# Kernel tuning notes

Hardware: AMD Instinct MI355X
Metric: run time of the kernel (lower is better)

The kernel has to match this reference:

```python
import jax, jax.numpy as jnp
import numpy as np

B, N, D = 4, 2048, 512
H, DH = 8, 64
MLP = 2048
EPS = 1e-5


def setup_inputs() -> dict:
    key = jax.random.key(0)
    ks = jax.random.split(key, 8)
    s = lambda fan_in: 1.0 / np.sqrt(fan_in)
    return {
        "x": jax.random.normal(ks[0], (B, N, D), jnp.float32),
        "ln1_g": jnp.ones((D,), jnp.float32),
        "ln1_b": jnp.zeros((D,), jnp.float32),
        "Wqkv": jax.random.normal(ks[1], (D, 3 * H * DH), jnp.float32) * s(D),
        "temperature": jnp.asarray(np.log(DH ** -0.5), jnp.float32),
        "Wo": jax.random.normal(ks[2], (H * DH, D), jnp.float32) * s(H * DH),
        "bo": jnp.zeros((D,), jnp.float32),
        "ln2_g": jnp.ones((D,), jnp.float32),
        "ln2_b": jnp.zeros((D,), jnp.float32),
        "W1": jax.random.normal(ks[3], (D, MLP), jnp.float32) * s(D),
        "b1": jnp.zeros((MLP,), jnp.float32),
        "W2": jax.random.normal(ks[4], (MLP, D), jnp.float32) * s(MLP),
        "b2": jnp.zeros((D,), jnp.float32),
    }


def _layernorm(x, g, b):
    mu = jnp.mean(x, axis=-1, keepdims=True)
    var = jnp.var(x, axis=-1, keepdims=True)
    return (x - mu) * jax.lax.rsqrt(var + EPS) * g + b


def _lsa(x, Wqkv, temperature, Wo, bo):
    b, n, _ = x.shape
    qkv = x @ Wqkv  # [b, n, 3*H*DH]
    q, k, v = jnp.split(qkv, 3, axis=-1)
    rs = lambda t: t.reshape(b, n, H, DH).transpose(0, 2, 1, 3)  # b h n d
    q, k, v = rs(q), rs(k), rs(v)
    dots = jnp.einsum("bhnd,bhmd->bhnm", q, k) * jnp.exp(temperature)
    mask_value = -jnp.finfo(dots.dtype).max
    eye = jnp.eye(n, dtype=bool)
    dots = jnp.where(eye, mask_value, dots)  # mask diagonal (LSA)
    attn = jax.nn.softmax(dots, axis=-1)
    out = jnp.einsum("bhnm,bhmd->bhnd", attn, v)
    out = out.transpose(0, 2, 1, 3).reshape(b, n, H * DH)
    return out @ Wo + bo


def _ffn(x, W1, b1, W2, b2):
    h = jax.nn.gelu(x @ W1 + b1, approximate=False)
    return h @ W2 + b2


def reference(x, ln1_g, ln1_b, Wqkv, temperature, Wo, bo,
              ln2_g, ln2_b, W1, b1, W2, b2):
    y = _lsa(_layernorm(x, ln1_g, ln1_b), Wqkv, temperature, Wo, bo) + x
    z = _ffn(_layernorm(y, ln2_g, ln2_b), W1, b1, W2, b2) + y
    return (z, x)
```

## Files before the change

### kernel.cpp

```cpp
#include <hip/hip_runtime.h>
#include <math.h>

typedef __attribute__((ext_vector_type(4))) float f32x4;
typedef __attribute__((ext_vector_type(8))) short short8;

#define DEV __device__ __forceinline__

DEV short f2bf(float f){
  union { float f; unsigned u; } v; v.f = f;
  unsigned r = v.u + 0x7fffu + ((v.u >> 16) & 1u);
  return (short)(r >> 16);
}
DEV float bf2f(short s){
  union { unsigned u; float f; } v; v.u = ((unsigned)(unsigned short)s) << 16; return v.f;
}
DEV float exp2_hw(float x){ float r; asm("v_exp_f32 %0, %1" : "=v"(r) : "v"(x)); return r; }
DEV float rcp_hw(float x){ float r; asm("v_rcp_f32 %0, %1" : "=v"(r) : "v"(x)); return r; }
DEV unsigned cvtpk(float a, float b){
  unsigned r; asm("v_cvt_pk_bf16_f32 %0, %1, %2" : "=v"(r) : "v"(a), "v"(b)); return r;
}
DEV void gload_lds16(const short* src, short* lds){
  __builtin_amdgcn_global_load_lds(
      (const __attribute__((address_space(1))) void*)src,
      (__attribute__((address_space(3))) void*)lds, 16, 0, 0);
}
DEV float gelu_fast(float v){
  float u = v * (0.79788456f + 0.03567741f * v * v);
  float e = exp2_hw(u * 2.88539008f);
  float th = 1.0f - 2.0f * rcp_hw(e + 1.0f);
  return 0.5f * v * (1.0f + th);
}

__global__ __launch_bounds__(256) void prep_kernel(
    const float* __restrict__ Wqkv, short* __restrict__ wqkv_t,
    const float* __restrict__ Wo,   short* __restrict__ wo_t,
    const float* __restrict__ W1,   short* __restrict__ w1_t,
    const float* __restrict__ W2,   short* __restrict__ w2_t,
    const float* __restrict__ x, const float* __restrict__ ln1g,
    const float* __restrict__ ln1b, short* __restrict__ h,
    float* __restrict__ xcopy)
{
  int bid = blockIdx.x;
  if (bid < 3072) {
    const float* W; short* Wt; int K, N, nbx, local;
    if (bid < 768)       { W = Wqkv; Wt = wqkv_t; K = 512;  N = 1536; nbx = 48; local = bid; }
    else if (bid < 1024) { W = Wo;   Wt = wo_t;   K = 512;  N = 512;  nbx = 16; local = bid - 768; }
    else if (bid < 2048) { W = W1;   Wt = w1_t;   K = 512;  N = 2048; nbx = 64; local = bid - 1024; }
    else                 { W = W2;   Wt = w2_t;   K = 2048; N = 512;  nbx = 16; local = bid - 2048; }
    __shared__ float tile[32][33];
    int nb = (local % nbx) * 32, kb = (local / nbx) * 32;
    int tx = threadIdx.x & 31, ty = threadIdx.x >> 5;
    #pragma unroll
    for (int i = ty; i < 32; i += 8)
      tile[i][tx] = W[(size_t)(kb + i) * N + nb + tx];
    __syncthreads();
    #pragma unroll
    for (int i = ty; i < 32; i += 8)
      Wt[(size_t)(nb + i) * K + kb + tx] = f2bf(tile[tx][i]);
    return;
  }
  int row  = (bid - 3072) * 4 + (threadIdx.x >> 6);
  int lane = threadIdx.x & 63;
  const float* xr = x + (size_t)row * 512 + lane * 8;
  f32x4 v0 = *(const f32x4*)(xr);
  f32x4 v1 = *(const f32x4*)(xr + 4);
  float s  = (v0[0]+v0[1]+v0[2]+v0[3]) + (v1[0]+v1[1]+v1[2]+v1[3]);
  float sq = (v0[0]*v0[0]+v0[1]*v0[1]+v0[2]*v0[2]+v0[3]*v0[3])
           + (v1[0]*v1[0]+v1[1]*v1[1]+v1[2]*v1[2]+v1[3]*v1[3]);
  #pragma unroll
  for (int off = 1; off < 64; off <<= 1) {
    s  += __shfl_xor(s, off);
    sq += __shfl_xor(sq, off);
  }
  float mu  = s * (1.0f / 512.0f);
  float var = sq * (1.0f / 512.0f) - mu * mu;
  float rstd = rsqrtf(var + 1e-5f);
  f32x4 g0 = *(const f32x4*)(ln1g + lane * 8);
  f32x4 g1 = *(const f32x4*)(ln1g + lane * 8 + 4);
  f32x4 b0 = *(const f32x4*)(ln1b + lane * 8);
  f32x4 b1 = *(const f32x4*)(ln1b + lane * 8 + 4);
  float o[8];
  #pragma unroll
  for (int j = 0; j < 4; ++j) o[j]     = (v0[j] - mu) * rstd * g0[j] + b0[j];
  #pragma unroll
  for (int j = 0; j < 4; ++j) o[4 + j] = (v1[j] - mu) * rstd * g1[j] + b1[j];
  uint4 pk;
  pk.x = cvtpk(o[0], o[1]); pk.y = cvtpk(o[2], o[3]);
  pk.z = cvtpk(o[4], o[5]); pk.w = cvtpk(o[6], o[7]);
  *(uint4*)(h + (size_t)row * 512 + lane * 8) = pk;
  float* xc = xcopy + (size_t)row * 512 + lane * 8;
  *(f32x4*)(xc)     = v0;
  *(f32x4*)(xc + 4) = v1;
}

__global__ __launch_bounds__(256) void ln_bf_kernel(
    const short* __restrict__ x, const float* __restrict__ g,
    const float* __restrict__ b, short* __restrict__ out)
{
  int row  = blockIdx.x * 4 + (threadIdx.x >> 6);
  int lane = threadIdx.x & 63;
  short8 raw = *(const short8*)(x + (size_t)row * 512 + lane * 8);
  float v[8];
  #pragma unroll
  for (int j = 0; j < 8; ++j) v[j] = bf2f(raw[j]);
  float s = 0.f, sq = 0.f;
  #pragma unroll
  for (int j = 0; j < 8; ++j) { s += v[j]; sq += v[j] * v[j]; }
  #pragma unroll
  for (int off = 1; off < 64; off <<= 1) {
    s  += __shfl_xor(s, off);
    sq += __shfl_xor(sq, off);
  }
  float mu  = s * (1.0f / 512.0f);
  float var = sq * (1.0f / 512.0f) - mu * mu;
  float rstd = rsqrtf(var + 1e-5f);
  f32x4 g0 = *(const f32x4*)(g + lane * 8);
  f32x4 g1 = *(const f32x4*)(g + lane * 8 + 4);
  f32x4 b0 = *(const f32x4*)(b + lane * 8);
  f32x4 b1 = *(const f32x4*)(b + lane * 8 + 4);
  float o[8];
  #pragma unroll
  for (int j = 0; j < 4; ++j) o[j]     = (v[j] - mu) * rstd * g0[j] + b0[j];
  #pragma unroll
  for (int j = 0; j < 4; ++j) o[4 + j] = (v[4+j] - mu) * rstd * g1[j] + b1[j];
  uint4 pk;
  pk.x = cvtpk(o[0], o[1]); pk.y = cvtpk(o[2], o[3]);
  pk.z = cvtpk(o[4], o[5]); pk.w = cvtpk(o[6], o[7]);
  *(uint4*)(out + (size_t)row * 512 + lane * 8) = pk;
}

template<int EPI, int BM, typename OutT>
__global__ __launch_bounds__(256) void gemm_bt_kernel(
    const short* __restrict__ A, const short* __restrict__ Bt,
    OutT* __restrict__ C, const float* __restrict__ bias,
    const float* __restrict__ resid, const short* __restrict__ residb,
    int M, int N, int K)
{
  constexpr int MFR = BM / 32;
  constexpr int NFR = 4;
  constexpr int AI  = BM / 32;
  constexpr int BUF = (BM + 128) * 64;
  __shared__ __align__(16) short smem[3 * BUF];

  int tid = threadIdx.x;
  int lane = tid & 63, wid = tid >> 6;
  int l16 = lane & 15, lq = lane >> 4;

  int gx = gridDim.x;
  int nwg = gx * gridDim.y;
  int orig = blockIdx.y * gx + blockIdx.x;
  int swz = (orig & 7) * (nwg >> 3) + (orig >> 3);
  int bn = swz % gx, bm = swz / gx;

  int wm = wid >> 1, wn = wid & 1;

  const short* gaP[AI];
  const short* gbP[4];
  #pragma unroll
  for (int i = 0; i < AI; ++i) {
    int g = i * 4 + wid;
    gaP[i] = A + (size_t)(bm * BM + (g >> 1) * 16 + l16) * K + (g & 1) * 32 + lq * 8;
  }
  #pragma unroll
  for (int i = 0; i < 4; ++i) {
    int g = i * 4 + wid;
    gbP[i] = Bt + (size_t)(bn * 128 + (g >> 1) * 16 + l16) * K + (g & 1) * 32 + lq * 8;
  }

  auto STAGE = [&](int bufi, int k0) {
    short* base = smem + bufi * BUF;
    #pragma unroll
    for (int i = 0; i < AI; ++i)
      gload_lds16(gaP[i] + k0, base + (i * 4 + wid) * 512);
    #pragma unroll
    for (int i = 0; i < 4; ++i)
      gload_lds16(gbP[i] + k0, base + BM * 64 + (i * 4 + wid) * 512);
  };

  f32x4 acc[MFR][NFR] = {};

  STAGE(0, 0);
  STAGE(1, 64);

  int nt = K >> 6;
  for (int t = 0; t < nt; ++t) {
    if (t + 1 < nt) asm volatile("s_waitcnt vmcnt(6)" ::: "memory");
    else            asm volatile("s_waitcnt vmcnt(0)" ::: "memory");
    __builtin_amdgcn_s_barrier();
    __builtin_amdgcn_sched_barrier(0);
    if (t + 2 < nt) STAGE((t + 2) % 3, (t + 2) << 6);

    const short* base = smem + (t % 3) * BUF;
    #pragma unroll
    for (int kc = 0; kc < 2; ++kc) {
      short8 af[MFR], bfr[NFR];
      #pragma unroll
      for (int m = 0; m < MFR; ++m)
        af[m] = *(const short8*)(base + ((wm * MFR + m) * 2 + kc) * 512 + lane * 8);
      #pragma unroll
      for (int n = 0; n < NFR; ++n)
        bfr[n] = *(const short8*)(base + BM * 64 + ((wn * NFR + n) * 2 + kc) * 512 + lane * 8);
      __builtin_amdgcn_s_setprio(1);
      #pragma unroll
      for (int m = 0; m < MFR; ++m)
        #pragma unroll
        for (int n = 0; n < NFR; ++n)
          acc[m][n] = __builtin_amdgcn_mfma_f32_16x16x32_bf16(af[m], bfr[n], acc[m][n], 0, 0, 0);
      __builtin_amdgcn_s_setprio(0);
    }
  }

  float bv[NFR];
  #pragma unroll
  for (int n = 0; n < NFR; ++n)
    bv[n] = bias[bn * 128 + (wn * NFR + n) * 16 + l16];

  #pragma unroll
  for (int m = 0; m < MFR; ++m) {
    #pragma unroll
    for (int r = 0; r < 4; ++r) {
      int row = bm * BM + (wm * MFR + m) * 16 + lq * 4 + r;
      #pragma unroll
      for (int n = 0; n < NFR; ++n) {
        int col = bn * 128 + (wn * NFR + n) * 16 + l16;
        float v = acc[m][n][r] + bv[n];
        if (EPI == 4) v += resid[(size_t)row * N + col];
        if (EPI == 5) v += bf2f(residb[(size_t)row * N + col]);
        if constexpr (sizeof(OutT) == 2)
          ((short*)C)[(size_t)row * N + col] = f2bf(v);
        else
          ((float*)C)[(size_t)row * N + col] = v;
      }
    }
  }
}

template<int EPI>
__global__ __launch_bounds__(512) void gemm256_kernel(
    const short* __restrict__ A, const short* __restrict__ Bt,
    short* __restrict__ C, const float* __restrict__ bias,
    short* __restrict__ vt, int M, int N, int K)
{
  constexpr int BUF = 24576;
  __shared__ __align__(16) short smem[3 * BUF];

  int tid = threadIdx.x;
  int lane = tid & 63, wid = tid >> 6;
  int l16 = lane & 15, lq = lane >> 4;

  int gx = gridDim.x;
  int nwg = gx * gridDim.y;
  int orig = blockIdx.y * gx + blockIdx.x;
  int swz = (orig & 7) * (nwg >> 3) + (orig >> 3);
  int bn = swz % gx, bm = swz / gx;

  int wm = wid >> 1, wn = wid & 1;

  const short* gaP[4];
  const short* gbP[2];
  #pragma unroll
  for (int i = 0; i < 4; ++i) {
    int g = i * 8 + wid;
    gaP[i] = A + (size_t)(bm * 256 + (g >> 1) * 16 + l16) * K + (g & 1) * 32 + lq * 8;
  }
  #pragma unroll
  for (int i = 0; i < 2; ++i) {
    int g = i * 8 + wid;
    gbP[i] = Bt + (size_t)(bn * 128 + (g >> 1) * 16 + l16) * K + (g & 1) * 32 + lq * 8;
  }

  auto STAGE = [&](int bufi, int k0) {
    short* base = smem + bufi * BUF;
    #pragma unroll
    for (int i = 0; i < 4; ++i)
      gload_lds16(gaP[i] + k0, base + (i * 8 + wid) * 512);
    #pragma unroll
    for (int i = 0; i < 2; ++i)
      gload_lds16(gbP[i] + k0, base + 16384 + (i * 8 + wid) * 512);
  };

  f32x4 acc[4][4] = {};

  STAGE(0, 0);
  STAGE(1, 64);

  int nt = K >> 6;
  for (int t = 0; t < nt; ++t) {
    if (t + 1 < nt) asm volatile("s_waitcnt vmcnt(6)" ::: "memory");
    else            asm volatile("s_waitcnt vmcnt(0)" ::: "memory");
    __builtin_amdgcn_s_barrier();
    __builtin_amdgcn_sched_barrier(0);
    if (t + 2 < nt) STAGE((t + 2) % 3, (t + 2) << 6);

    const short* base = smem + (t % 3) * BUF;
    #pragma unroll
    for (int kc = 0; kc < 2; ++kc) {
      short8 af[4], bfr[4];
      #pragma unroll
      for (int m = 0; m < 4; ++m)
        af[m] = *(const short8*)(base + ((wm * 4 + m) * 2 + kc) * 512 + lane * 8);
      #pragma unroll
      for (int n = 0; n < 4; ++n)
        bfr[n] = *(const short8*)(base + 16384 + ((wn * 4 + n) * 2 + kc) * 512 + lane * 8);
      __builtin_amdgcn_s_setprio(1);
      #pragma unroll
      for (int m = 0; m < 4; ++m)
        #pragma unroll
        for (int n = 0; n < 4; ++n)
          acc[m][n] = __builtin_amdgcn_mfma_f32_16x16x32_bf16(af[m], bfr[n], acc[m][n], 0, 0, 0);
      __builtin_amdgcn_s_setprio(0);
    }
  }

  if (EPI == 3 && bn >= 8) {
    __syncthreads();
    short* T = smem;
    #pragma unroll
    for (int m = 0; m < 4; ++m)
      #pragma unroll
      for (int n = 0; n < 4; ++n) {
        int c = wn * 64 + n * 16 + l16;
        #pragma unroll
        for (int r = 0; r < 4; ++r) {
          int rowl = wm * 64 + m * 16 + lq * 4 + r;
          T[c * 256 + (rowl ^ ((c & 7) << 4))] = f2bf(acc[m][n][r]);
        }
      }
    __syncthreads();
    int b2 = bm >> 3;
    int nnb = (bm & 7) * 256;
    int tn = tid & 31, cw = tid >> 5;
    #pragma unroll
    for (int c8 = 0; c8 < 8; ++c8) {
      int c = c8 * 16 + cw;
      short8 v = *(const short8*)(T + c * 256 + ((tn * 8) ^ ((c & 7) << 4)));
      if (tn & 1) {
        short8 w;
        #pragma unroll
        for (int j = 0; j < 8; ++j) w[j] = v[j ^ 4];
        v = w;
      }
      int c2 = bn * 128 + c - 1024;
      int bh = b2 * 8 + (c2 >> 6);
      int d  = c2 & 63;
      *(short8*)(vt + ((size_t)(bh * 64 + d)) * 2048 + nnb + tn * 8) = v;
    }
    return;
  }

  #pragma unroll
  for (int m = 0; m < 4; ++m) {
    #pragma unroll
    for (int r = 0; r < 4; ++r) {
      int row = bm * 256 + (wm * 4 + m) * 16 + lq * 4 + r;
      #pragma unroll
      for (int n = 0; n < 4; ++n) {
        int col = bn * 128 + (wn * 4 + n) * 16 + l16;
        C[(size_t)row * N + col] = f2bf(acc[m][n][r]);
      }
    }
  }
}

__global__ __launch_bounds__(512, 2) void gemm8p_kernel(
    const short* __restrict__ A, const short* __restrict__ Bt,
    short* __restrict__ C, const float* __restrict__ bias,
    int M, int N, int K)
{
  __shared__ __align__(16) short smem[2 * 32768];

  int tid = threadIdx.x;
  int lane = tid & 63, wid = tid >> 6;
  int l16 = lane & 15, lq = lane >> 4;
  int wm = wid >> 2, wn = wid & 3;

  int gx = gridDim.x;
  int nwg = gx * gridDim.y;
  int orig = blockIdx.y * gx + blockIdx.x;
  int swz = (orig & 7) * (nwg >> 3) + (orig >> 3);
  int bn = swz % gx, bm = swz / gx;

  const short* gaP[4];
  const short* gbP[4];
  #pragma unroll
  for (int i = 0; i < 4; ++i) {
    int idx = i * 512 + tid;
    int g = idx >> 6, ln = idx & 63;
    gaP[i] = A  + (size_t)(bm * 256 + (g >> 1) * 16 + (ln & 15)) * K
                + (g & 1) * 32 + (ln >> 4) * 8;
    gbP[i] = Bt + (size_t)(bn * 256 + (g >> 1) * 16 + (ln & 15)) * K
                + (g & 1) * 32 + (ln >> 4) * 8;
  }

  auto STAGE_A = [&](int buf, int k0) {
    short* dst = smem + buf * 32768;
    #pragma unroll
    for (int i = 0; i < 4; ++i)
      gload_lds16(gaP[i] + k0, dst + ((size_t)(i * 512 + tid)) * 8);
  };
  auto STAGE_B_LO = [&](int buf, int k0) {
    short* dst = smem + buf * 32768 + 16384;
    #pragma unroll
    for (int i = 0; i < 2; ++i)
      gload_lds16(gbP[i] + k0, dst + ((size_t)(i * 512 + tid)) * 8);
  };
  auto STAGE_B_HI = [&](int buf, int k0) {
    short* dst = smem + buf * 32768 + 16384;
    #pragma unroll
    for (int i = 2; i < 4; ++i)
      gload_lds16(gbP[i] + k0, dst + ((size_t)(i * 512 + tid)) * 8);
  };

  f32x4 acc[8][4] = {};

  STAGE_A(0, 0);
  STAGE_B_LO(0, 0); STAGE_B_HI(0, 0);
  STAGE_B_LO(1, 64); STAGE_B_HI(1, 64);
  asm volatile("s_waitcnt vmcnt(4)" ::: "memory");
  __builtin_amdgcn_s_barrier();

  int nt = K >> 6;
  for (int t = 0; t < nt; ++t) {
    int cur = t & 1;
    const short* As_ = smem + cur * 32768;
    const short* Bs_ = As_ + 16384;
    short8 bf[4][2];

    #pragma unroll
    for (int p = 0; p < 4; ++p) {
      short8 af[2][2];
      #pragma unroll
      for (int mm = 0; mm < 2; ++mm)
        #pragma unroll
        for (int kc = 0; kc < 2; ++kc)
          af[mm][kc] = *(const short8*)(As_ + ((wm * 8 + 2 * p + mm) * 2 + kc) * 512 + lane * 8);
      if (p == 0) {
        #pragma unroll
        for (int n = 0; n < 4; ++n)
          #pragma unroll
          for (int kc = 0; kc < 2; ++kc)
            bf[n][kc] = *(const short8*)(Bs_ + ((wn * 4 + n) * 2 + kc) * 512 + lane * 8);
      }
      if (p == 0 && t + 1 < nt) STAGE_A(cur ^ 1, (t + 1) << 6);
      if (p == 1 && t + 2 < nt) STAGE_B_LO(cur, (t + 2) << 6);
      if (p == 2 && t + 2 < nt) STAGE_B_HI(cur, (t + 2) << 6);

      __builtin_amdgcn_s_barrier();
      asm volatile("s_waitcnt lgkmcnt(0)" ::: "memory");
      __builtin_amdgcn_sched_barrier(0);
      __builtin_amdgcn_s_setprio(1);
      #pragma unroll
      for (int mm = 0; mm < 2; ++mm)
        #pragma unroll
        for (int n = 0; n < 4; ++n)
          #pragma unroll
          for (int kc = 0; kc < 2; ++kc)
            acc[2 * p + mm][n] = __builtin_amdgcn_mfma_f32_16x16x32_bf16(
                af[mm][kc], bf[n][kc], acc[2 * p + mm][n], 0, 0, 0);
      __builtin_amdgcn_s_setprio(0);
      if (p < 3) {
        __builtin_amdgcn_s_barrier();
      } else {
        if (t + 2 < nt) asm volatile("s_waitcnt vmcnt(4)" ::: "memory");
        else            asm volatile("s_waitcnt vmcnt(0)" ::: "memory");
        __builtin_amdgcn_s_barrier();
      }
    }
  }

  float bv[4];
  #pragma unroll
  for (int n = 0; n < 4; ++n)
    bv[n] = bias[bn * 256 + (wn * 4 + n) * 16 + l16];
  #pragma unroll
  for (int m = 0; m < 8; ++m) {
    #pragma unroll
    for (int r = 0; r < 4; ++r) {
      int row = bm * 256 + wm * 128 + m * 16 + lq * 4 + r;
      #pragma unroll
      for (int n = 0; n < 4; ++n) {
        int col = bn * 256 + (wn * 4 + n) * 16 + l16;
        C[(size_t)row * N + col] = f2bf(gelu_fast(acc[m][n][r] + bv[n]));
      }
    }
  }
}

__global__ __launch_bounds__(512, 4) void attn_kernel(
    const short* __restrict__ qkv, const short* __restrict__ vt,
    const float* __restrict__ temp_ptr,
    short* __restrict__ Op0, short* __restrict__ Op1, float* __restrict__ Lbuf)
{
  __shared__ __align__(16) short smem[16384];

  int tid = threadIdx.x;
  int lane = tid & 63, wid = tid >> 6;
  int l16 = lane & 15, lq = lane >> 4;
  int hi = lq >> 1, lq0 = lq & 1;

  int orig = blockIdx.y * 8 + blockIdx.x;
  int swz = (orig & 7) * 64 + (orig >> 3);
  int qb = swz & 7;
  int rr = swz >> 3;
  int bh = rr & 31, slice = rr >> 5;
  int b = bh >> 3, h = bh & 7;

  const short* qbase = qkv + (size_t)b * 2048 * 1536 + h * 64;
  const short* kbase = qbase + 512;
  const short* vbase = vt + (size_t)bh * 64 * 2048;
  int kslice = slice * 1024;

  float scale = __expf(temp_ptr[0]) * 1.44269504f;
  int q0 = qb * 256 + wid * 32;

  short8 qfrag[2][2];
  #pragma unroll
  for (int qf = 0; qf < 2; ++qf) {
    int qrow = q0 + qf * 16 + l16;
    #pragma unroll
    for (int c = 0; c < 2; ++c) {
      short8 raw = *(const short8*)(qbase + (size_t)qrow * 1536 + c * 32 + lq * 8);
      short8 sc;
      #pragma unroll
      for (int j = 0; j < 8; ++j) sc[j] = f2bf(bf2f(raw[j]) * scale);
      qfrag[qf][c] = sc;
    }
  }

  f32x4 accO[2][4] = {};
  float l[2] = {0.f, 0.f};

  auto STAGE = [&](int bufi, int k0) {
    int sub = wid >> 1, cc = wid & 1;
    const short* srcK = kbase + (size_t)(k0 + sub * 16 + l16) * 1536 + cc * 32 + lq * 8;
    gload_lds16(srcK, smem + bufi * 4096 + wid * 512);
    const short* srcV = vbase + (size_t)(sub * 16 + l16) * 2048 + k0 + cc * 32 + lq * 8;
    gload_lds16(srcV, smem + 8192 + bufi * 4096 + wid * 512);
  };

  STAGE(0, kslice);
  asm volatile("s_waitcnt vmcnt(0)");
  __syncthreads();

  for (int t = 0; t < 16; ++t) {
    int cur = t & 1;
    int k0 = kslice + t * 64;
    if (t + 1 < 16) STAGE(cur ^ 1, k0 + 64);

    const short* kls = smem + cur * 4096;
    const short* vls = smem + 8192 + cur * 4096;

    f32x4 accS[2][4] = {};
    #pragma unroll
    for (int s = 0; s < 4; ++s) {
      short8 kf0 = *(const short8*)(kls + (s * 2 + 0) * 512 + lane * 8);
      short8 kf1 = *(const short8*)(kls + (s * 2 + 1) * 512 + lane * 8);
      #pragma unroll
      for (int qf = 0; qf < 2; ++qf) {
        accS[qf][s] = __builtin_amdgcn_mfma_f32_16x16x32_bf16(kf0, qfrag[qf][0], accS[qf][s], 0, 0, 0);
        accS[qf][s] = __builtin_amdgcn_mfma_f32_16x16x32_bf16(kf1, qfrag[qf][1], accS[qf][s], 0, 0, 0);
      }
    }

    if ((q0 & ~63) == k0) {
      #pragma unroll
      for (int qf = 0; qf < 2; ++qf) {
        int qg = q0 + qf * 16 + l16;
        #pragma unroll
        for (int s = 0; s < 4; ++s)
          #pragma unroll
          for (int r = 0; r < 4; ++r)
            if (k0 + s * 16 + lq * 4 + r == qg) accS[qf][s][r] = -30000.f;
      }
    }

    short8 pa[2][2];
    #pragma unroll
    for (int qf = 0; qf < 2; ++qf) {
      float sum = 0.f;
      unsigned W[4][2];
      #pragma unroll
      for (int s = 0; s < 4; ++s) {
        float p0 = exp2_hw(accS[qf][s][0]);
        float p1 = exp2_hw(accS[qf][s][1]);
        float p2 = exp2_hw(accS[qf][s][2]);
        float p3 = exp2_hw(accS[qf][s][3]);
        sum += (p0 + p1) + (p2 + p3);
        W[s][0] = cvtpk(p0, p1);
        W[s][1] = cvtpk(p2, p3);
      }
      sum += __shfl_xor(sum, 16);
      sum += __shfl_xor(sum, 32);
      l[qf] += sum;

      unsigned K0[2], S0[2], K2[2], S2[2], R0[2], R2[2];
      #pragma unroll
      for (int w = 0; w < 2; ++w) {
        K0[w] = hi ? W[1][w] : W[0][w];
        S0[w] = hi ? W[0][w] : W[1][w];
        K2[w] = hi ? W[3][w] : W[2][w];
        S2[w] = hi ? W[2][w] : W[3][w];
      }
      #pragma unroll
      for (int w = 0; w < 2; ++w) {
        R0[w] = (unsigned)__shfl_xor((int)S0[w], 32);
        R2[w] = (unsigned)__shfl_xor((int)S2[w], 32);
      }
      bool sw = (hi != lq0);
      unsigned FA[2], FB[2], sA[2], sB[2], GA[2], GB[2];
      #pragma unroll
      for (int w = 0; w < 2; ++w) {
        sA[w] = sw ? K0[w] : R0[w];  FA[w] = sw ? R0[w] : K0[w];
        sB[w] = sw ? K2[w] : R2[w];  FB[w] = sw ? R2[w] : K2[w];
      }
      #pragma unroll
      for (int w = 0; w < 2; ++w) {
        GA[w] = (unsigned)__shfl_xor((int)sA[w], 16);
        GB[w] = (unsigned)__shfl_xor((int)sB[w], 16);
      }
      union { unsigned u[4]; short8 s8; } p0u, p1u;
      p0u.u[0] = FA[0]; p0u.u[1] = FA[1]; p0u.u[2] = GA[0]; p0u.u[3] = GA[1];
      p1u.u[0] = FB[0]; p1u.u[1] = FB[1]; p1u.u[2] = GB[0]; p1u.u[3] = GB[1];
      pa[qf][0] = p0u.s8;
      pa[qf][1] = p1u.s8;
    }

    short8 vfr[4][2];
    #pragma unroll
    for (int d = 0; d < 4; ++d) {
      vfr[d][0] = *(const short8*)(vls + (d * 2 + 0) * 512 + lane * 8);
      vfr[d][1] = *(const short8*)(vls + (d * 2 + 1) * 512 + lane * 8);
    }
    #pragma unroll
    for (int qf = 0; qf < 2; ++qf)
      #pragma unroll
      for (int d = 0; d < 4; ++d) {
        accO[qf][d] = __builtin_amdgcn_mfma_f32_16x16x32_bf16(vfr[d][0], pa[qf][0], accO[qf][d], 0, 0, 0);
        accO[qf][d] = __builtin_amdgcn_mfma_f32_16x16x32_bf16(vfr[d][1], pa[qf][1], accO[qf][d], 0, 0, 0);
      }

    __syncthreads();
  }

  short* op = slice ? Op1 : Op0;
  #pragma unroll
  for (int qf = 0; qf < 2; ++qf) {
    int qg = q0 + qf * 16 + l16;
    if (lq == 0) Lbuf[(size_t)(slice * 32 + bh) * 2048 + qg] = l[qf];
    size_t rowoff = (size_t)(b * 2048 + qg) * 512 + h * 64;
    #pragma unroll
    for (int d = 0; d < 4; ++d) {
      unsigned w0 = cvtpk(accO[qf][d][0], accO[qf][d][1]);
      unsigned w1 = cvtpk(accO[qf][d][2], accO[qf][d][3]);
      uint2 pk; pk.x = w0; pk.y = w1;
      *(uint2*)(op + rowoff + d * 16 + lq * 4) = pk;
    }
  }
}

__global__ __launch_bounds__(256) void attn_combine_kernel(
    const short* __restrict__ Op0, const short* __restrict__ Op1,
    const float* __restrict__ Lbuf, short* __restrict__ out)
{
  int idx = blockIdx.x * 256 + threadIdx.x;
  size_t e = (size_t)idx * 8;
  int row = (int)(e >> 9);
  int col = (int)(e & 511);
  int b = row >> 11, q = row & 2047;
  int bh = b * 8 + (col >> 6);
  float l0 = Lbuf[(size_t)bh * 2048 + q];
  float l1 = Lbuf[(size_t)(32 + bh) * 2048 + q];
  float inv = rcp_hw(l0 + l1);
  short8 a = *(const short8*)(Op0 + e);
  short8 c = *(const short8*)(Op1 + e);
  float o[8];
  #pragma unroll
  for (int j = 0; j < 8; ++j) o[j] = (bf2f(a[j]) + bf2f(c[j])) * inv;
  uint4 pk;
  pk.x = cvtpk(o[0], o[1]); pk.y = cvtpk(o[2], o[3]);
  pk.z = cvtpk(o[4], o[5]); pk.w = cvtpk(o[6], o[7]);
  *(uint4*)(out + e) = pk;
}

extern "C" void kernel_launch(void* const* d_in, const int* in_sizes, int n_in,
                              void* d_out, int out_size, void* d_ws, size_t ws_size,
                              hipStream_t stream)
{
  const float* x    = (const float*)d_in[0];
  const float* ln1g = (const float*)d_in[1];
  const float* ln1b = (const float*)d_in[2];
  const float* Wqkv = (const float*)d_in[3];
  const float* temp = (const float*)d_in[4];
  const float* Wo   = (const float*)d_in[5];
  const float* bo   = (const float*)d_in[6];
  const float* ln2g = (const float*)d_in[7];
  const float* ln2b = (const float*)d_in[8];
  const float* W1   = (const float*)d_in[9];
  const float* b1   = (const float*)d_in[10];
  const float* W2   = (const float*)d_in[11];
  const float* b2   = (const float*)d_in[12];
  float* out = (float*)d_out;

  char* ws = (char*)d_ws;
  short* wqkv_t = (short*)(ws);
  float* lpart  = (float*)(ws);
  short* wo_t   = (short*)(ws + 1572864);
  short* w1_t   = (short*)(ws + 2097152);
  short* w2_t   = (short*)(ws + 4194304);
  short* h      = (short*)(ws + 6291456);
  short* qkv    = (short*)(ws + 14680064);
  short* attn   = (short*)(ws + 39845888);
  short* ybf    = (short*)(ws + 48234496);
  short* vt     = (short*)(ws + 48234496);
  short* t      = (short*)(ws + 14680064);

  const int M = 8192;

  prep_kernel<<<3072 + 2048, 256, 0, stream>>>(
      Wqkv, wqkv_t, Wo, wo_t, W1, w1_t, W2, w2_t,
      x, ln1g, ln1b, h, out + (size_t)M * 512);

  gemm256_kernel<3><<<dim3(1536 / 128, M / 256), 512, 0, stream>>>(
      h, wqkv_t, qkv, nullptr, vt, M, 1536, 512);

  attn_kernel<<<dim3(8, 64), 512, 0, stream>>>(qkv, vt, temp, attn, h, lpart);
  attn_combine_kernel<<<M * 512 / 8 / 256, 256, 0, stream>>>(attn, h, lpart, attn);

  gemm_bt_kernel<4, 64, short><<<dim3(512 / 128, M / 64), 256, 0, stream>>>(
      attn, wo_t, ybf, bo, x, nullptr, M, 512, 512);

  ln_bf_kernel<<<M / 4, 256, 0, stream>>>(ybf, ln2g, ln2b, h);

  gemm8p_kernel<<<dim3(2048 / 256, M / 256), 512, 0, stream>>>(
      h, w1_t, t, b1, M, 2048, 512);

  gemm_bt_kernel<5, 64, float><<<dim3(512 / 128, M / 64), 256, 0, stream>>>(
      t, w2_t, out, b2, nullptr, ybf, M, 512, 2048);
}
```

Before: 191.8 us.

## Use 256x256 GEMM for QKV and split attention keys into four slices

The QKV projection now runs through the templated 256x256 eight-phase GEMM, which writes V transposed through its LDS epilogue, instead of the separate 256x128 kernel. Attention splits the key range into four slices instead of two, doubling the grid so more blocks stay resident per CU. The fourth partial output is stored in the now-unused V columns of the qkv buffer, and the combine kernel sums four partials. The trade-offs are that the QKV GEMM grid shrinks to 192 blocks, which may underfill the GPU, and the combine step now reads twice as much partial data.

```diff
diff --git a/kernel.cpp b/kernel.cpp
--- a/kernel.cpp
+++ b/kernel.cpp
@@ -235,137 +235,11 @@
   }
 }
 
-template<int EPI>
-__global__ __launch_bounds__(512) void gemm256_kernel(
+template<int QKV>
+__global__ __launch_bounds__(512, 2) void gemm8p_kernel(
     const short* __restrict__ A, const short* __restrict__ Bt,
     short* __restrict__ C, const float* __restrict__ bias,
     short* __restrict__ vt, int M, int N, int K)
-{
-  constexpr int BUF = 24576;
-  __shared__ __align__(16) short smem[3 * BUF];
-
-  int tid = threadIdx.x;
-  int lane = tid & 63, wid = tid >> 6;
-  int l16 = lane & 15, lq = lane >> 4;
-
-  int gx = gridDim.x;
-  int nwg = gx * gridDim.y;
-  int orig = blockIdx.y * gx + blockIdx.x;
-  int swz = (orig & 7) * (nwg >> 3) + (orig >> 3);
-  int bn = swz % gx, bm = swz / gx;
-
-  int wm = wid >> 1, wn = wid & 1;
-
-  const short* gaP[4];
-  const short* gbP[2];
-  #pragma unroll
-  for (int i = 0; i < 4; ++i) {
-    int g = i * 8 + wid;
-    gaP[i] = A + (size_t)(bm * 256 + (g >> 1) * 16 + l16) * K + (g & 1) * 32 + lq * 8;
-  }
-  #pragma unroll
-  for (int i = 0; i < 2; ++i) {
-    int g = i * 8 + wid;
-    gbP[i] = Bt + (size_t)(bn * 128 + (g >> 1) * 16 + l16) * K + (g & 1) * 32 + lq * 8;
-  }
-
-  auto STAGE = [&](int bufi, int k0) {
-    short* base = smem + bufi * BUF;
-    #pragma unroll
-    for (int i = 0; i < 4; ++i)
-      gload_lds16(gaP[i] + k0, base + (i * 8 + wid) * 512);
-    #pragma unroll
-    for (int i = 0; i < 2; ++i)
-      gload_lds16(gbP[i] + k0, base + 16384 + (i * 8 + wid) * 512);
-  };
-
-  f32x4 acc[4][4] = {};
-
-  STAGE(0, 0);
-  STAGE(1, 64);
-
-  int nt = K >> 6;
-  for (int t = 0; t < nt; ++t) {
-    if (t + 1 < nt) asm volatile("s_waitcnt vmcnt(6)" ::: "memory");
-    else            asm volatile("s_waitcnt vmcnt(0)" ::: "memory");
-    __builtin_amdgcn_s_barrier();
-    __builtin_amdgcn_sched_barrier(0);
-    if (t + 2 < nt) STAGE((t + 2) % 3, (t + 2) << 6);
-
-    const short* base = smem + (t % 3) * BUF;
-    #pragma unroll
-    for (int kc = 0; kc < 2; ++kc) {
-      short8 af[4], bfr[4];
-      #pragma unroll
-      for (int m = 0; m < 4; ++m)
-        af[m] = *(const short8*)(base + ((wm * 4 + m) * 2 + kc) * 512 + lane * 8);
-      #pragma unroll
-      for (int n = 0; n < 4; ++n)
-        bfr[n] = *(const short8*)(base + 16384 + ((wn * 4 + n) * 2 + kc) * 512 + lane * 8);
-      __builtin_amdgcn_s_setprio(1);
-      #pragma unroll
-      for (int m = 0; m < 4; ++m)
-        #pragma unroll
-        for (int n = 0; n < 4; ++n)
-          acc[m][n] = __builtin_amdgcn_mfma_f32_16x16x32_bf16(af[m], bfr[n], acc[m][n], 0, 0, 0);
-      __builtin_amdgcn_s_setprio(0);
-    }
-  }
-
-  if (EPI == 3 && bn >= 8) {
-    __syncthreads();
-    short* T = smem;
-    #pragma unroll
-    for (int m = 0; m < 4; ++m)
-      #pragma unroll
-      for (int n = 0; n < 4; ++n) {
-        int c = wn * 64 + n * 16 + l16;
-        #pragma unroll
-        for (int r = 0; r < 4; ++r) {
-          int rowl = wm * 64 + m * 16 + lq * 4 + r;
-          T[c * 256 + (rowl ^ ((c & 7) << 4))] = f2bf(acc[m][n][r]);
-        }
-      }
-    __syncthreads();
-    int b2 = bm >> 3;
-    int nnb = (bm & 7) * 256;
-    int tn = tid & 31, cw = tid >> 5;
-    #pragma unroll
-    for (int c8 = 0; c8 < 8; ++c8) {
-      int c = c8 * 16 + cw;
-      short8 v = *(const short8*)(T + c * 256 + ((tn * 8) ^ ((c & 7) << 4)));
-      if (tn & 1) {
-        short8 w;
-        #pragma unroll
-        for (int j = 0; j < 8; ++j) w[j] = v[j ^ 4];
-        v = w;
-      }
-      int c2 = bn * 128 + c - 1024;
-      int bh = b2 * 8 + (c2 >> 6);
-      int d  = c2 & 63;
-      *(short8*)(vt + ((size_t)(bh * 64 + d)) * 2048 + nnb + tn * 8) = v;
-    }
-    return;
-  }
-
-  #pragma unroll
-  for (int m = 0; m < 4; ++m) {
-    #pragma unroll
-    for (int r = 0; r < 4; ++r) {
-      int row = bm * 256 + (wm * 4 + m) * 16 + lq * 4 + r;
-      #pragma unroll
-      for (int n = 0; n < 4; ++n) {
-        int col = bn * 128 + (wn * 4 + n) * 16 + l16;
-        C[(size_t)row * N + col] = f2bf(acc[m][n][r]);
-      }
-    }
-  }
-}
-
-__global__ __launch_bounds__(512, 2) void gemm8p_kernel(
-    const short* __restrict__ A, const short* __restrict__ Bt,
-    short* __restrict__ C, const float* __restrict__ bias,
-    int M, int N, int K)
 {
   __shared__ __align__(16) short smem[2 * 32768];
 
@@ -468,10 +342,48 @@
     }
   }
 
+  if (QKV == 1 && bn >= 4) {
+    __syncthreads();
+    short* T = smem;
+    #pragma unroll
+    for (int m = 0; m < 8; ++m)
+      #pragma unroll
+      for (int n = 0; n < 4; ++n) {
+        int c = (wn * 4 + n) * 16 + l16;
+        #pragma unroll
+        for (int r = 0; r < 4; ++r) {
+          int rowl = wm * 128 + m * 16 + lq * 4 + r;
+          T[c * 256 + (rowl ^ ((c & 7) << 4))] = f2bf(acc[m][n][r]);
+        }
+      }
+    __syncthreads();
+    int b2 = bm >> 3;
+    int nnb = (bm & 7) * 256;
+    int tn = tid & 31, cw = tid >> 5;
+    #pragma unroll
+    for (int c8 = 0; c8 < 16; ++c8) {
+      int c = c8 * 16 + cw;
+      short8 v = *(const short8*)(T + c * 256 + ((tn * 8) ^ ((c & 7) << 4)));
+      if (tn & 1) {
+        short8 w;
+        #pragma unroll
+        for (int j = 0; j < 8; ++j) w[j] = v[j ^ 4];
+        v = w;
+      }
+      int c2 = bn * 256 + c - 1024;
+      int bh = b2 * 8 + (c2 >> 6);
+      int d  = c2 & 63;
+      *(short8*)(vt + ((size_t)(bh * 64 + d)) * 2048 + nnb + tn * 8) = v;
+    }
+    return;
+  }
+
   float bv[4];
-  #pragma unroll
-  for (int n = 0; n < 4; ++n)
-    bv[n] = bias[bn * 256 + (wn * 4 + n) * 16 + l16];
+  if (QKV == 0) {
+    #pragma unroll
+    for (int n = 0; n < 4; ++n)
+      bv[n] = bias[bn * 256 + (wn * 4 + n) * 16 + l16];
+  }
   #pragma unroll
   for (int m = 0; m < 8; ++m) {
     #pragma unroll
@@ -480,7 +392,9 @@
       #pragma unroll
       for (int n = 0; n < 4; ++n) {
         int col = bn * 256 + (wn * 4 + n) * 16 + l16;
-        C[(size_t)row * N + col] = f2bf(gelu_fast(acc[m][n][r] + bv[n]));
+        float v = acc[m][n][r];
+        if (QKV == 0) v = gelu_fast(v + bv[n]);
+        C[(size_t)row * N + col] = f2bf(v);
       }
     }
   }
@@ -489,7 +403,8 @@
 __global__ __launch_bounds__(512, 4) void attn_kernel(
     const short* __restrict__ qkv, const short* __restrict__ vt,
     const float* __restrict__ temp_ptr,
-    short* __restrict__ Op0, short* __restrict__ Op1, float* __restrict__ Lbuf)
+    short* __restrict__ Op0, short* __restrict__ Op1, short* __restrict__ Op2,
+    short* __restrict__ qkvw, float* __restrict__ Lbuf)
 {
   __shared__ __align__(16) short smem[16384];
 
@@ -499,7 +414,7 @@
   int hi = lq >> 1, lq0 = lq & 1;
 
   int orig = blockIdx.y * 8 + blockIdx.x;
-  int swz = (orig & 7) * 64 + (orig >> 3);
+  int swz = (orig & 7) * 128 + (orig >> 3);
   int qb = swz & 7;
   int rr = swz >> 3;
   int bh = rr & 31, slice = rr >> 5;
@@ -508,7 +423,7 @@
   const short* qbase = qkv + (size_t)b * 2048 * 1536 + h * 64;
   const short* kbase = qbase + 512;
   const short* vbase = vt + (size_t)bh * 64 * 2048;
-  int kslice = slice * 1024;
+  int kslice = slice * 512;
 
   float scale = __expf(temp_ptr[0]) * 1.44269504f;
   int q0 = qb * 256 + wid * 32;
@@ -542,10 +457,10 @@
   asm volatile("s_waitcnt vmcnt(0)");
   __syncthreads();
 
-  for (int t = 0; t < 16; ++t) {
+  for (int t = 0; t < 8; ++t) {
     int cur = t & 1;
     int k0 = kslice + t * 64;
-    if (t + 1 < 16) STAGE(cur ^ 1, k0 + 64);
+    if (t + 1 < 8) STAGE(cur ^ 1, k0 + 64);
 
     const short* kls = smem + cur * 4096;
     const short* vls = smem + 8192 + cur * 4096;
@@ -642,24 +557,28 @@
     __syncthreads();
   }
 
-  short* op = slice ? Op1 : Op0;
   #pragma unroll
   for (int qf = 0; qf < 2; ++qf) {
     int qg = q0 + qf * 16 + l16;
     if (lq == 0) Lbuf[(size_t)(slice * 32 + bh) * 2048 + qg] = l[qf];
-    size_t rowoff = (size_t)(b * 2048 + qg) * 512 + h * 64;
     #pragma unroll
     for (int d = 0; d < 4; ++d) {
       unsigned w0 = cvtpk(accO[qf][d][0], accO[qf][d][1]);
       unsigned w1 = cvtpk(accO[qf][d][2], accO[qf][d][3]);
       uint2 pk; pk.x = w0; pk.y = w1;
-      *(uint2*)(op + rowoff + d * 16 + lq * 4) = pk;
+      if (slice < 3) {
+        short* op = (slice == 0) ? Op0 : (slice == 1) ? Op1 : Op2;
+        *(uint2*)(op + (size_t)(b * 2048 + qg) * 512 + h * 64 + d * 16 + lq * 4) = pk;
+      } else {
+        *(uint2*)(qkvw + (size_t)(b * 2048 + qg) * 1536 + 1024 + h * 64 + d * 16 + lq * 4) = pk;
+      }
     }
   }
 }
 
 __global__ __launch_bounds__(256) void attn_combine_kernel(
     const short* __restrict__ Op0, const short* __restrict__ Op1,
+    const short* __restrict__ Op2, const short* __restrict__ Op3q,
     const float* __restrict__ Lbuf, short* __restrict__ out)
 {
   int idx = blockIdx.x * 256 + threadIdx.x;
@@ -670,12 +589,17 @@
   int bh = b * 8 + (col >> 6);
   float l0 = Lbuf[(size_t)bh * 2048 + q];
   float l1 = Lbuf[(size_t)(32 + bh) * 2048 + q];
-  float inv = rcp_hw(l0 + l1);
-  short8 a = *(const short8*)(Op0 + e);
-  short8 c = *(const short8*)(Op1 + e);
+  float l2 = Lbuf[(size_t)(64 + bh) * 2048 + q];
+  float l3 = Lbuf[(size_t)(96 + bh) * 2048 + q];
+  float inv = rcp_hw(l0 + l1 + l2 + l3);
+  short8 a0 = *(const short8*)(Op0 + e);
+  short8 a1 = *(const short8*)(Op1 + e);
+  short8 a2 = *(const short8*)(Op2 + e);
+  short8 a3 = *(const short8*)(Op3q + (size_t)row * 1536 + 1024 + col);
   float o[8];
   #pragma unroll
-  for (int j = 0; j < 8; ++j) o[j] = (bf2f(a[j]) + bf2f(c[j])) * inv;
+  for (int j = 0; j < 8; ++j)
+    o[j] = (bf2f(a0[j]) + bf2f(a1[j]) + bf2f(a2[j]) + bf2f(a3[j])) * inv;
   uint4 pk;
   pk.x = cvtpk(o[0], o[1]); pk.y = cvtpk(o[2], o[3]);
   pk.z = cvtpk(o[4], o[5]); pk.w = cvtpk(o[6], o[7]);
@@ -712,6 +636,7 @@
   short* attn   = (short*)(ws + 39845888);
   short* ybf    = (short*)(ws + 48234496);
   short* vt     = (short*)(ws + 48234496);
+  short* op2    = (short*)(ws + 56623104);
   short* t      = (short*)(ws + 14680064);
 
   const int M = 8192;
@@ -720,19 +645,19 @@
       Wqkv, wqkv_t, Wo, wo_t, W1, w1_t, W2, w2_t,
       x, ln1g, ln1b, h, out + (size_t)M * 512);
 
-  gemm256_kernel<3><<<dim3(1536 / 128, M / 256), 512, 0, stream>>>(
+  gemm8p_kernel<1><<<dim3(1536 / 256, M / 256), 512, 0, stream>>>(
       h, wqkv_t, qkv, nullptr, vt, M, 1536, 512);
 
-  attn_kernel<<<dim3(8, 64), 512, 0, stream>>>(qkv, vt, temp, attn, h, lpart);
-  attn_combine_kernel<<<M * 512 / 8 / 256, 256, 0, stream>>>(attn, h, lpart, attn);
+  attn_kernel<<<dim3(8, 128), 512, 0, stream>>>(qkv, vt, temp, attn, h, op2, qkv, lpart);
+  attn_combine_kernel<<<M * 512 / 8 / 256, 256, 0, stream>>>(attn, h, op2, qkv, lpart, attn);
 
   gemm_bt_kernel<4, 64, short><<<dim3(512 / 128, M / 64), 256, 0, stream>>>(
       attn, wo_t, ybf, bo, x, nullptr, M, 512, 512);
 
   ln_bf_kernel<<<M / 4, 256, 0, stream>>>(ybf, ln2g, ln2b, h);
 
-  gemm8p_kernel<<<dim3(2048 / 256, M / 256), 512, 0, stream>>>(
-      h, w1_t, t, b1, M, 2048, 512);
+  gemm8p_kernel<0><<<dim3(2048 / 256, M / 256), 512, 0, stream>>>(
+      h, w1_t, t, b1, nullptr, M, 2048, 512);
 
   gemm_bt_kernel<5, 64, float><<<dim3(512 / 128, M / 64), 256, 0, stream>>>(
       t, w2_t, out, b2, nullptr, ybf, M, 512, 2048);
```

Result: no change. 194.4 us (+1.3%).
